# Performance work log

Measured on AMD Instinct MI355X. Metric: run time of the kernel, lower is better.

Reference implementation:

```python
import jax, jax.numpy as jnp
import numpy as np

EPS = 1e-5  # torch InstanceNorm3d default eps


def setup_inputs() -> dict:
    key = jax.random.key(0)
    kx, kw, kb = jax.random.split(key, 3)
    # x: (B, C_in, T, D, H, W)
    x = jax.random.normal(kx, (1, 4, 8, 96, 96, 96), dtype=jnp.float32)
    # 4D hypercube conv kernel: (C_out, C_in, kT, kD, kH, kW)
    w = jax.random.normal(kw, (8, 4, 3, 3, 3, 3), dtype=jnp.float32) * 0.05
    b = jax.random.normal(kb, (8,), dtype=jnp.float32) * 0.05
    return {"x": x, "w": w, "b": b}


def reference(x, w, b):
    # Per-time-slice InstanceNorm3d (affine=False): normalizing each t-slice
    # over (D,H,W) per (b,c) is identical to normalizing over spatial dims
    # per (b,c,t) in one fused pass (the torch loop + stack is just this).
    mean = jnp.mean(x, axis=(3, 4, 5), keepdims=True)
    var = jnp.var(x, axis=(3, 4, 5), keepdims=True)  # biased, as in torch
    xn = (x - mean) * jax.lax.rsqrt(var + EPS)
    # ReLU activation
    xa = jax.nn.relu(xn)
    # True 4D convolution (T,D,H,W spatial), padding=1 everywhere, stride 1.
    # This equals the repo's Conv4d (sum of per-temporal-offset Conv3d's).
    out = jax.lax.conv_general_dilated(
        xa, w,
        window_strides=(1, 1, 1, 1),
        padding=[(1, 1)] * 4,
        dimension_numbers=("NCTDHW", "OITDHW", "NCTDHW"),
    )
    return out + b.reshape(1, -1, 1, 1, 1, 1)
```

## Files before the change

kernel.cpp:

```cpp
#include <hip/hip_runtime.h>

#define CI 4
#define CO 8
#define TT 8
#define S 96
#define SLICE (S*S*S)
#define NSLICE (CI*TT)
#define EPS 1e-5f


__global__ __launch_bounds__(256) void stats_partial(
        const float* __restrict__ x, float* __restrict__ ws) {
    const int slice = blockIdx.y;
    const float4* p = reinterpret_cast<const float4*>(x + (size_t)slice * SLICE);
    const int n4 = SLICE / 4;
    float s = 0.f, ss = 0.f;
    for (int i = blockIdx.x * blockDim.x + threadIdx.x; i < n4;
         i += gridDim.x * blockDim.x) {
        float4 v = p[i];
        s  += v.x + v.y + v.z + v.w;
        ss += v.x*v.x + v.y*v.y + v.z*v.z + v.w*v.w;
    }
    #pragma unroll
    for (int off = 32; off > 0; off >>= 1) {
        s  += __shfl_down(s, off);
        ss += __shfl_down(ss, off);
    }
    __shared__ float ls[4], lss[4];
    const int lane = threadIdx.x & 63, wid = threadIdx.x >> 6;
    if (lane == 0) { ls[wid] = s; lss[wid] = ss; }
    __syncthreads();
    if (threadIdx.x == 0) {
        float ts  = ls[0] + ls[1] + ls[2] + ls[3];
        float tss = lss[0] + lss[1] + lss[2] + lss[3];
        atomicAdd(&ws[slice], ts);
        atomicAdd(&ws[NSLICE + slice], tss);
    }
}

__global__ __launch_bounds__(192, 3) void conv4d_fused(
        const float* __restrict__ x, const float* __restrict__ wgt,
        const float* __restrict__ bias, const float* __restrict__ ws,
        float* __restrict__ out) {
    const int lane = threadIdx.x;
    const int ty   = threadIdx.y;
    const int w0   = lane << 2;
    const int d    = blockIdx.x;
    const int h0   = (blockIdx.y * 8 + ty) * 2;
    const int t    = blockIdx.z;

    float acc[2][CO][4];
    #pragma unroll
    for (int p = 0; p < 2; p++)
        #pragma unroll
        for (int co = 0; co < CO; co++)
            #pragma unroll
            for (int j = 0; j < 4; j++) acc[p][co][j] = 0.f;

    const bool wlb = (lane > 0), wrb = (lane < 23);
    const int  om1 = wlb ? -1 : 0;
    const int  op4 = wrb ?  4 : 3;
    const float fwl = wlb ? 1.f : 0.f, fwr = wrb ? 1.f : 0.f;
    const float inv_n = 1.f / (float)SLICE;

    for (int ci = 0; ci < CI; ci++) {
        for (int kt = 0; kt < 3; kt++) {
            const int tt = t + kt - 1;
            if ((unsigned)tt >= TT) continue;
            const int sl = ci * TT + tt;
            const float mean = ws[sl] * inv_n;
            const float var  = ws[NSLICE + sl] * inv_n - mean * mean;
            const float rstd = rsqrtf(var + EPS);
            const float nmr  = -mean * rstd;
            const float* xs = x + (size_t)sl * SLICE;
            #pragma unroll
            for (int kd = 0; kd < 3; kd++) {
                const int dd = d + kd - 1;
                const float md = ((unsigned)dd < S) ? 1.f : 0.f;
                const int dc = dd < 0 ? 0 : (dd > S - 1 ? S - 1 : dd);
                const float* xp = xs + (size_t)dc * (S * S);
                const float* wb = wgt + (ci * 3 + kt) * 27 + kd * 9;

                float n[4][6];
                #pragma unroll
                for (int r = 0; r < 4; r++) {
                    const int hh = h0 + r - 1;
                    const float m_ = (((unsigned)hh < S) ? 1.f : 0.f) * md;
                    const int hc = hh < 0 ? 0 : (hh > S - 1 ? S - 1 : hh);
                    const float* row = xp + hc * S + w0;
                    const float4 f4 = *reinterpret_cast<const float4*>(row);
                    const float e0 = row[om1];
                    const float e1 = row[op4];
                    const float rs = rstd * m_, nm = nmr * m_;
                    n[r][0] = fwl * fmaxf(fmaf(e0,   rs, nm), 0.f);
                    n[r][1] =       fmaxf(fmaf(f4.x, rs, nm), 0.f);
                    n[r][2] =       fmaxf(fmaf(f4.y, rs, nm), 0.f);
                    n[r][3] =       fmaxf(fmaf(f4.z, rs, nm), 0.f);
                    n[r][4] =       fmaxf(fmaf(f4.w, rs, nm), 0.f);
                    n[r][5] = fwr * fmaxf(fmaf(e1,   rs, nm), 0.f);
                }

                #define TAP(P, KH, NR) do {                                   \
                    const float* wp_ = wb + (KH) * 3;                         \
                    _Pragma("unroll")                                         \
                    for (int co = 0; co < CO; co++) {                         \
                        const float* wc_ = wp_ + co * (CI * 81);              \
                        const float k0 = wc_[0], k1 = wc_[1], k2 = wc_[2];    \
                        _Pragma("unroll")                                     \
                        for (int j = 0; j < 4; j++) {                         \
                            acc[P][co][j] = fmaf(NR[j],     k0, acc[P][co][j]);\
                            acc[P][co][j] = fmaf(NR[j + 1], k1, acc[P][co][j]);\
                            acc[P][co][j] = fmaf(NR[j + 2], k2, acc[P][co][j]);\
                        }                                                     \
                    }                                                         \
                } while (0)

                TAP(0, 0, n[0]);
                TAP(0, 1, n[1]); TAP(1, 0, n[1]);
                TAP(0, 2, n[2]); TAP(1, 1, n[2]);
                TAP(1, 2, n[3]);
                #undef TAP
            }
        }
    }

    #pragma unroll
    for (int p = 0; p < 2; p++) {
        const size_t obase = (((size_t)t * S + d) * S + (h0 + p)) * S + w0;
        #pragma unroll
        for (int co = 0; co < CO; co++) {
            const float bb = bias[co];
            float4 o;
            o.x = acc[p][co][0] + bb;
            o.y = acc[p][co][1] + bb;
            o.z = acc[p][co][2] + bb;
            o.w = acc[p][co][3] + bb;
            *reinterpret_cast<float4*>(out + (size_t)co * ((size_t)TT * SLICE) + obase) = o;
        }
    }
}

extern "C" void kernel_launch(void* const* d_in, const int* in_sizes, int n_in,
                              void* d_out, int out_size, void* d_ws, size_t ws_size,
                              hipStream_t stream) {
    const float* x   = (const float*)d_in[0];
    const float* w   = (const float*)d_in[1];
    const float* b   = (const float*)d_in[2];
    float* out = (float*)d_out;
    float* ws  = (float*)d_ws;

    hipMemsetAsync(ws, 0, 2 * NSLICE * sizeof(float), stream);
    stats_partial<<<dim3(64, NSLICE), 256, 0, stream>>>(x, ws);
    conv4d_fused<<<dim3(S, S / 16, TT), dim3(24, 8, 1), 0, stream>>>(x, w, b, ws, out);
}
```

Baseline: 699.7 us.

## Software-pipeline depth-slice row loads and transpose weights for contiguous scalar access

The conv kernel now loads the input rows for the next depth slice into a second register buffer before the current slice is computed, so global load latency can overlap with the FMAs. A small pre-kernel rewrites the weights into a (ci,kt,kd,kh,co,kw) layout in the workspace, so each tap's 24 weights sit together and can be fetched with fewer scalar loads. The FMA loop is also reordered so each weight triple feeds both output rows. The extra register buffers may increase register pressure under the 3-blocks-per-SM launch bound, and the transpose adds one more launch.

Result: slower. 787.6 us (+12.6%).

```diff
diff --git a/kernel.cpp b/kernel.cpp
--- a/kernel.cpp
+++ b/kernel.cpp
@@ -7,6 +7,8 @@
 #define SLICE (S*S*S)
 #define NSLICE (CI*TT)
 #define EPS 1e-5f
+#define WTOT (CO*CI*81)
+#define WS_WT_OFF 64
 
 
 __global__ __launch_bounds__(256) void stats_partial(
@@ -38,8 +40,77 @@
     }
 }
 
+__global__ void wtranspose(const float* __restrict__ w, float* __restrict__ wt) {
+    int i = blockIdx.x * blockDim.x + threadIdx.x;
+    if (i >= WTOT) return;
+    int kw = i % 3; int r = i / 3;
+    int co = r % CO; r /= CO;
+    int kh = r % 3;  r /= 3;
+    int kd = r % 3;  r /= 3;
+    int kt = r % 3;  r /= 3;
+    int ci = r;
+    wt[i] = w[((((co * CI + ci) * 3 + kt) * 3 + kd) * 3 + kh) * 3 + kw];
+}
+
+__device__ __forceinline__ void load_rows(
+        const float* __restrict__ xp, int h0, int w0, int om1, int op4,
+        float4 f4[4], float e0[4], float e1[4]) {
+    #pragma unroll
+    for (int r = 0; r < 4; r++) {
+        const int hh = h0 + r - 1;
+        const int hc = hh < 0 ? 0 : (hh > S - 1 ? S - 1 : hh);
+        const float* row = xp + hc * S + w0;
+        f4[r] = *reinterpret_cast<const float4*>(row);
+        e0[r] = row[om1];
+        e1[r] = row[op4];
+    }
+}
+
+template <bool TW>
+__device__ __forceinline__ void compute_kd(
+        const float4 f4[4], const float e0[4], const float e1[4],
+        float rstd, float nmr, float md, int h0, float fwl, float fwr,
+        const float* __restrict__ wp, float acc[2][CO][4]) {
+    float n[4][6];
+    #pragma unroll
+    for (int r = 0; r < 4; r++) {
+        const int hh = h0 + r - 1;
+        const float m_ = (((unsigned)hh < S) ? 1.f : 0.f) * md;
+        const float rs = rstd * m_, nm = nmr * m_;
+        n[r][0] = fwl * fmaxf(fmaf(e0[r],   rs, nm), 0.f);
+        n[r][1] =       fmaxf(fmaf(f4[r].x, rs, nm), 0.f);
+        n[r][2] =       fmaxf(fmaf(f4[r].y, rs, nm), 0.f);
+        n[r][3] =       fmaxf(fmaf(f4[r].z, rs, nm), 0.f);
+        n[r][4] =       fmaxf(fmaf(f4[r].w, rs, nm), 0.f);
+        n[r][5] = fwr * fmaxf(fmaf(e1[r],   rs, nm), 0.f);
+    }
+    #pragma unroll
+    for (int kh = 0; kh < 3; kh++) {
+        #pragma unroll
+        for (int co = 0; co < CO; co++) {
+            const float* wc = TW ? (wp + kh * 24 + co * 3)
+                                 : (wp + co * (CI * 81) + kh * 3);
+            const float k0 = wc[0], k1 = wc[1], k2 = wc[2];
+            #pragma unroll
+            for (int j = 0; j < 4; j++) {
+                float a0 = acc[0][co][j];
+                a0 = fmaf(n[kh][j],     k0, a0);
+                a0 = fmaf(n[kh][j + 1], k1, a0);
+                a0 = fmaf(n[kh][j + 2], k2, a0);
+                acc[0][co][j] = a0;
+                float a1 = acc[1][co][j];
+                a1 = fmaf(n[kh + 1][j],     k0, a1);
+                a1 = fmaf(n[kh + 1][j + 1], k1, a1);
+                a1 = fmaf(n[kh + 1][j + 2], k2, a1);
+                acc[1][co][j] = a1;
+            }
+        }
+    }
+}
+
+template <bool TW>
 __global__ __launch_bounds__(192, 3) void conv4d_fused(
-        const float* __restrict__ x, const float* __restrict__ wgt,
+        const float* __restrict__ x, const float* __restrict__ wsrc,
         const float* __restrict__ bias, const float* __restrict__ ws,
         float* __restrict__ out) {
     const int lane = threadIdx.x;
@@ -62,6 +133,14 @@
     const int  op4 = wrb ?  4 : 3;
     const float fwl = wlb ? 1.f : 0.f, fwr = wrb ? 1.f : 0.f;
     const float inv_n = 1.f / (float)SLICE;
+
+    const int dm1 = d > 0 ? d - 1 : 0;
+    const int dp1 = d < S - 1 ? d + 1 : S - 1;
+    const float md0 = d > 0 ? 1.f : 0.f;
+    const float md2 = d < S - 1 ? 1.f : 0.f;
+
+    float4 fA[4], fB[4];
+    float eA0[4], eA1[4], eB0[4], eB1[4];
 
     for (int ci = 0; ci < CI; ci++) {
         for (int kt = 0; kt < 3; kt++) {
@@ -73,54 +152,21 @@
             const float rstd = rsqrtf(var + EPS);
             const float nmr  = -mean * rstd;
             const float* xs = x + (size_t)sl * SLICE;
-            #pragma unroll
-            for (int kd = 0; kd < 3; kd++) {
-                const int dd = d + kd - 1;
-                const float md = ((unsigned)dd < S) ? 1.f : 0.f;
-                const int dc = dd < 0 ? 0 : (dd > S - 1 ? S - 1 : dd);
-                const float* xp = xs + (size_t)dc * (S * S);
-                const float* wb = wgt + (ci * 3 + kt) * 27 + kd * 9;
-
-                float n[4][6];
-                #pragma unroll
-                for (int r = 0; r < 4; r++) {
-                    const int hh = h0 + r - 1;
-                    const float m_ = (((unsigned)hh < S) ? 1.f : 0.f) * md;
-                    const int hc = hh < 0 ? 0 : (hh > S - 1 ? S - 1 : hh);
-                    const float* row = xp + hc * S + w0;
-                    const float4 f4 = *reinterpret_cast<const float4*>(row);
-                    const float e0 = row[om1];
-                    const float e1 = row[op4];
-                    const float rs = rstd * m_, nm = nmr * m_;
-                    n[r][0] = fwl * fmaxf(fmaf(e0,   rs, nm), 0.f);
-                    n[r][1] =       fmaxf(fmaf(f4.x, rs, nm), 0.f);
-                    n[r][2] =       fmaxf(fmaf(f4.y, rs, nm), 0.f);
-                    n[r][3] =       fmaxf(fmaf(f4.z, rs, nm), 0.f);
-                    n[r][4] =       fmaxf(fmaf(f4.w, rs, nm), 0.f);
-                    n[r][5] = fwr * fmaxf(fmaf(e1,   rs, nm), 0.f);
-                }
-
-                #define TAP(P, KH, NR) do {                                   \
-                    const float* wp_ = wb + (KH) * 3;                         \
-                    _Pragma("unroll")                                         \
-                    for (int co = 0; co < CO; co++) {                         \
-                        const float* wc_ = wp_ + co * (CI * 81);              \
-                        const float k0 = wc_[0], k1 = wc_[1], k2 = wc_[2];    \
-                        _Pragma("unroll")                                     \
-                        for (int j = 0; j < 4; j++) {                         \
-                            acc[P][co][j] = fmaf(NR[j],     k0, acc[P][co][j]);\
-                            acc[P][co][j] = fmaf(NR[j + 1], k1, acc[P][co][j]);\
-                            acc[P][co][j] = fmaf(NR[j + 2], k2, acc[P][co][j]);\
-                        }                                                     \
-                    }                                                         \
-                } while (0)
-
-                TAP(0, 0, n[0]);
-                TAP(0, 1, n[1]); TAP(1, 0, n[1]);
-                TAP(0, 2, n[2]); TAP(1, 1, n[2]);
-                TAP(1, 2, n[3]);
-                #undef TAP
-            }
+            const float* xp0 = xs + (size_t)dm1 * (S * S);
+            const float* xp1 = xs + (size_t)d   * (S * S);
+            const float* xp2 = xs + (size_t)dp1 * (S * S);
+            const float* wp = TW ? (wsrc + (ci * 3 + kt) * 216)
+                                 : (wsrc + ci * 81 + kt * 27);
+
+            load_rows(xp0, h0, w0, om1, op4, fA, eA0, eA1);
+            load_rows(xp1, h0, w0, om1, op4, fB, eB0, eB1);
+            compute_kd<TW>(fA, eA0, eA1, rstd, nmr, md0, h0, fwl, fwr,
+                           TW ? wp : wp, acc);
+            load_rows(xp2, h0, w0, om1, op4, fA, eA0, eA1);
+            compute_kd<TW>(fB, eB0, eB1, rstd, nmr, 1.f, h0, fwl, fwr,
+                           TW ? wp + 72 : wp + 9, acc);
+            compute_kd<TW>(fA, eA0, eA1, rstd, nmr, md2, h0, fwl, fwr,
+                           TW ? wp + 144 : wp + 18, acc);
         }
     }
 
@@ -149,7 +195,16 @@
     float* out = (float*)d_out;
     float* ws  = (float*)d_ws;
 
+    const bool tw = ws_size >= (size_t)(WS_WT_OFF + WTOT) * sizeof(float);
+
     hipMemsetAsync(ws, 0, 2 * NSLICE * sizeof(float), stream);
     stats_partial<<<dim3(64, NSLICE), 256, 0, stream>>>(x, ws);
-    conv4d_fused<<<dim3(S, S / 16, TT), dim3(24, 8, 1), 0, stream>>>(x, w, b, ws, out);
-}
+    if (tw) {
+        wtranspose<<<(WTOT + 255) / 256, 256, 0, stream>>>(w, ws + WS_WT_OFF);
+        conv4d_fused<true><<<dim3(S, S / 16, TT), dim3(24, 8, 1), 0, stream>>>(
+                x, ws + WS_WT_OFF, b, ws, out);
+    } else {
+        conv4d_fused<false><<<dim3(S, S / 16, TT), dim3(24, 8, 1), 0, stream>>>(
+                x, w, b, ws, out);
+    }
+}
```
